# Performance work log

Measured on AMD Instinct MI355X. Metric: run time of the kernel, lower is better.

The kernel has to match this reference:

```python
import jax, jax.numpy as jnp
import numpy as np

LN_EPS = 1e-5  # torch nn.LayerNorm default


def _layernorm(h):
    # elementwise_affine=False LayerNorm over last dim
    mu = jnp.mean(h, axis=-1, keepdims=True)
    var = jnp.var(h, axis=-1, keepdims=True)
    return (h - mu) * jax.lax.rsqrt(var + LN_EPS)


def setup_inputs() -> dict:
    key = jax.random.key(0)
    ks = jax.random.split(key, 7)
    B, M, D, L = 10240, 8, 512, 3  # b=1024*10 and m=8 are hardcoded in the module
    rn = lambda k, shape, scale=1.0: jax.random.normal(k, shape, dtype=jnp.float32) * scale
    return {
        "x":   rn(ks[0], (B, D)),
        "Ws":  rn(ks[1], (L, M, D, D), 0.05),  # per-layer basis weight tensors (m,i,j)
        "bs":  rn(ks[2], (L, M, D), 0.05),     # per-layer basis biases (m,i)
        "pWs": rn(ks[3], (L, B, M)),           # per-sample weight-mixing coeffs
        "pbs": rn(ks[4], (L, B, M)),           # per-sample bias-mixing coeffs
        "gWs": rn(ks[5], (L, B, D, 1)),        # gates (squeezed in forward)
        "gbs": rn(ks[6], (L, B, D)),
    }


def reference(x, Ws, bs, pWs, pbs, gWs, gbs):
    L = Ws.shape[0]
    for l in range(L):
        gW = gWs[l][..., 0]                                  # (b, i)
        # 'bi,bm,mij,bj->bi' without materializing (b,i,j):
        y = jnp.einsum('mij,bj->bmi', Ws[l], x)              # (b, m, i)
        Wx = gW * jnp.einsum('bm,bmi->bi', pWs[l], y)        # (b, i)
        # 'bj,bm,mj->bj' (bias lives in output dim)
        bias = gbs[l] * jnp.einsum('bm,mi->bi', pbs[l], bs[l])
        h = Wx + bias
        if l != L - 1:  # hidden layers: LayerNorm (no affine) + ELU; last: identity
            h = jax.nn.elu(_layernorm(h))
        x = h
    return x
```

## Files before the change

kernel.cpp:

```cpp
#include <hip/hip_runtime.h>
#include <math.h>

#define BB   10240
#define DD   512
#define MM   8

typedef _Float16 h8 __attribute__((ext_vector_type(8)));
typedef float    f4 __attribute__((ext_vector_type(4)));

__device__ __forceinline__ void gload16(const void* g, void* l) {
    __builtin_amdgcn_global_load_lds(
        (__attribute__((address_space(1))) void*)(g),
        (__attribute__((address_space(3))) void*)(l), 16, 0, 0);
}

__global__ void __launch_bounds__(256) cvt_f32_f16(const float* __restrict__ s,
                                                   _Float16* __restrict__ d, int n8) {
    int i = blockIdx.x * 256 + threadIdx.x;
    if (i >= n8) return;
    const float4* sp = (const float4*)s + (size_t)i * 2;
    float4 a = sp[0], b = sp[1];
    h8 o = { (_Float16)a.x, (_Float16)a.y, (_Float16)a.z, (_Float16)a.w,
             (_Float16)b.x, (_Float16)b.y, (_Float16)b.z, (_Float16)b.w };
    *(h8*)(d + (size_t)i * 8) = o;
}

template <int HALF_OUT>
__global__ void __launch_bounds__(256, 3) gemm_layer(
    const _Float16* __restrict__ xh,
    const _Float16* __restrict__ Wh,
    const float*  __restrict__ pW,
    const float*  __restrict__ pb,
    const float*  __restrict__ bsv,
    const float*  __restrict__ gW,
    const float*  __restrict__ gb,
    float* __restrict__ outf,
    _Float16* __restrict__ outh)
{
    __shared__ __align__(16) _Float16 Wl[4][3][32 * 64];

    const int tid  = threadIdx.x;
    const int lane = tid & 63;
    const int w    = tid >> 6;
    const int wm   = w >> 1, wn = w & 1;
    const int ln16 = lane & 15, quad = lane >> 4;
    const int bn0  = blockIdx.x * 64;
    const int bm0  = blockIdx.y * 128;

    _Float16 pwh[4][8];
    #pragma unroll
    for (int mt = 0; mt < 4; ++mt) {
        const float* pp = pW + (size_t)(bm0 + wm * 64 + mt * 16 + ln16) * MM;
        float4 p0 = *(const float4*)pp;
        float4 p1 = *(const float4*)(pp + 4);
        pwh[mt][0] = (_Float16)p0.x; pwh[mt][1] = (_Float16)p0.y;
        pwh[mt][2] = (_Float16)p0.z; pwh[mt][3] = (_Float16)p0.w;
        pwh[mt][4] = (_Float16)p1.x; pwh[mt][5] = (_Float16)p1.y;
        pwh[mt][6] = (_Float16)p1.z; pwh[mt][7] = (_Float16)p1.w;
    }

    const _Float16* ab0 = xh + (size_t)(bm0 + wm * 64 + ln16) * DD + quad * 8;

    f4 acc[4][2] = {};
    h8 afr[2][4], afn[2][4];

#define STW(S_, M_, JC_) do {                                                  \
    _Pragma("unroll")                                                          \
    for (int c = 0; c < 4; ++c) {                                              \
        int rit     = c * 8 + (lane >> 3);             \
        int logical = (lane & 7) ^ (lane >> 3);           \
        const _Float16* gp = Wh + (size_t)(M_) * (DD * DD)                     \
                               + (size_t)(bn0 + wn * 32 + rit) * DD            \
                               + (JC_) * 64 + logical * 8;                     \
        gload16(gp, &Wl[w][S_][c * 512]);                                      \
    }                                                                          \
} while (0)

#define AL(DST, JC) do {                                                       \
    _Pragma("unroll")                                                          \
    for (int _ks = 0; _ks < 2; ++_ks)                                          \
        _Pragma("unroll")                                                      \
        for (int _mt = 0; _mt < 4; ++_mt)                                      \
            DST[_ks][_mt] = *(const h8*)(ab0 + (size_t)_mt * (16 * DD)         \
                                         + (size_t)(JC) * 64 + _ks * 32);      \
} while (0)

#define GS(T_, N_, CUR, NXT, DOA) do {                                         \
    if ((T_) + 2 <= 63) STW((((T_) + 2) % 3), (((T_) + 2) & 7),                \
                            (((T_) + 2) >> 3));                                \
    if (DOA) AL(NXT, ((T_) >> 3) + 1);                                         \
    asm volatile("s_waitcnt vmcnt(%0)" :: "i"(N_) : "memory");                 \
    __builtin_amdgcn_sched_barrier(0);                                         \
    h8 wfr[2][2];                                                              \
    _Pragma("unroll")                                                          \
    for (int ks = 0; ks < 2; ++ks)                                             \
        _Pragma("unroll")                                                      \
        for (int nt = 0; nt < 2; ++nt) {                                       \
            int row  = nt * 16 + ln16;                                         \
            int phys = (ks * 4 + quad) ^ (ln16 & 7);                           \
            wfr[ks][nt] = *(const h8*)&Wl[w][(T_) % 3][row * 64 + phys * 8];   \
        }                                                                      \
    _Pragma("unroll")                                                          \
    for (int ks = 0; ks < 2; ++ks)                                             \
        _Pragma("unroll")                                                      \
        for (int mt = 0; mt < 4; ++mt) {                                       \
            h8 as = CUR[ks][mt] * pwh[mt][(T_) & 7];      \
            acc[mt][0] = __builtin_amdgcn_mfma_f32_16x16x32_f16(               \
                as, wfr[ks][0], acc[mt][0], 0, 0, 0);                          \
            acc[mt][1] = __builtin_amdgcn_mfma_f32_16x16x32_f16(               \
                as, wfr[ks][1], acc[mt][1], 0, 0, 0);                          \
        }                                                                      \
} while (0)

    AL(afr, 0);
    STW(0, 0, 0);
    STW(1, 1, 0);

    GS( 0,  8, afr, afn, 0);            
    GS( 1,  8, afr, afn, 0);
    GS( 2,  8, afr, afn, 0);
    GS( 3, 16, afr, afn, 1);
    GS( 4, 16, afr, afn, 0);
    GS( 5, 16, afr, afn, 0);
    GS( 6,  8, afr, afn, 0);
    GS( 7,  8, afr, afn, 0);
    GS( 8,  8, afn, afr, 0);
    GS( 9,  8, afn, afr, 0);
    GS(10,  8, afn, afr, 0);
    GS(11, 16, afn, afr, 1);
    GS(12, 16, afn, afr, 0);
    GS(13, 16, afn, afr, 0);
    GS(14,  8, afn, afr, 0);
    GS(15,  8, afn, afr, 0);
    GS(16,  8, afr, afn, 0);
    GS(17,  8, afr, afn, 0);
    GS(18,  8, afr, afn, 0);
    GS(19, 16, afr, afn, 1);
    GS(20, 16, afr, afn, 0);
    GS(21, 16, afr, afn, 0);
    GS(22,  8, afr, afn, 0);
    GS(23,  8, afr, afn, 0);
    GS(24,  8, afn, afr, 0);
    GS(25,  8, afn, afr, 0);
    GS(26,  8, afn, afr, 0);
    GS(27, 16, afn, afr, 1);
    GS(28, 16, afn, afr, 0);
    GS(29, 16, afn, afr, 0);
    GS(30,  8, afn, afr, 0);
    GS(31,  8, afn, afr, 0);
    GS(32,  8, afr, afn, 0);
    GS(33,  8, afr, afn, 0);
    GS(34,  8, afr, afn, 0);
    GS(35, 16, afr, afn, 1);
    GS(36, 16, afr, afn, 0);
    GS(37, 16, afr, afn, 0);
    GS(38,  8, afr, afn, 0);
    GS(39,  8, afr, afn, 0);
    GS(40,  8, afn, afr, 0);
    GS(41,  8, afn, afr, 0);
    GS(42,  8, afn, afr, 0);
    GS(43, 16, afn, afr, 1);
    GS(44, 16, afn, afr, 0);
    GS(45, 16, afn, afr, 0);
    GS(46,  8, afn, afr, 0);
    GS(47,  8, afn, afr, 0);
    GS(48,  8, afr, afn, 0);
    GS(49,  8, afr, afn, 0);
    GS(50,  8, afr, afn, 0);
    GS(51, 16, afr, afn, 1);
    GS(52, 16, afr, afn, 0);
    GS(53, 16, afr, afn, 0);
    GS(54,  8, afr, afn, 0);
    GS(55,  8, afr, afn, 0);
    GS(56,  8, afn, afr, 0);
    GS(57,  8, afn, afr, 0);
    GS(58,  8, afn, afr, 0);
    GS(59,  8, afn, afr, 0);
    GS(60,  8, afn, afr, 0);
    GS(61,  8, afn, afr, 0);
    GS(62,  4, afn, afr, 0);
    GS(63,  0, afn, afr, 0);

#undef GS
#undef AL
#undef STW

    const int i0 = bn0 + wn * 32 + ln16;
    const int i1 = i0 + 16;
    float bs0[8], bs1[8];
    #pragma unroll
    for (int m2 = 0; m2 < 8; ++m2) {
        bs0[m2] = bsv[m2 * DD + i0];
        bs1[m2] = bsv[m2 * DD + i1];
    }
    #pragma unroll
    for (int mt = 0; mt < 4; ++mt) {
        #pragma unroll
        for (int r = 0; r < 4; ++r) {
            int b = bm0 + wm * 64 + mt * 16 + quad * 4 + r;
            float4 p0 = *(const float4*)(pb + (size_t)b * MM);
            float4 p1 = *(const float4*)(pb + (size_t)b * MM + 4);
            float bias0 = p0.x*bs0[0] + p0.y*bs0[1] + p0.z*bs0[2] + p0.w*bs0[3]
                        + p1.x*bs0[4] + p1.y*bs0[5] + p1.z*bs0[6] + p1.w*bs0[7];
            float bias1 = p0.x*bs1[0] + p0.y*bs1[1] + p0.z*bs1[2] + p0.w*bs1[3]
                        + p1.x*bs1[4] + p1.y*bs1[5] + p1.z*bs1[6] + p1.w*bs1[7];
            float v0 = gW[(size_t)b * DD + i0] * acc[mt][0][r] + gb[(size_t)b * DD + i0] * bias0;
            float v1 = gW[(size_t)b * DD + i1] * acc[mt][1][r] + gb[(size_t)b * DD + i1] * bias1;
            if (HALF_OUT) {
                outh[(size_t)b * DD + i0] = (_Float16)v0;
                outh[(size_t)b * DD + i1] = (_Float16)v1;
            } else {
                outf[(size_t)b * DD + i0] = v0;
                outf[(size_t)b * DD + i1] = v1;
            }
        }
    }
}

__global__ void __launch_bounds__(256) ln_elu_h(const _Float16* __restrict__ h,
                                                _Float16* __restrict__ xo) {
    const int w    = threadIdx.x >> 6;
    const int lane = threadIdx.x & 63;
    const int row  = blockIdx.x * 4 + w;
    h8 v = *(const h8*)(h + (size_t)row * DD + lane * 8);
    float f[8], s = 0.f, q = 0.f;
    #pragma unroll
    for (int i = 0; i < 8; ++i) { f[i] = (float)v[i]; s += f[i]; q += f[i] * f[i]; }
    #pragma unroll
    for (int off = 1; off < 64; off <<= 1) {
        s += __shfl_xor(s, off);
        q += __shfl_xor(q, off);
    }
    float mu   = s * (1.0f / 512.0f);
    float var  = q * (1.0f / 512.0f) - mu * mu;
    float rstd = rsqrtf(var + 1e-5f);
    h8 o;
    #pragma unroll
    for (int i = 0; i < 8; ++i) {
        float t = (f[i] - mu) * rstd;
        t = t > 0.0f ? t : expm1f(t);
        o[i] = (_Float16)t;
    }
    *(h8*)(xo + (size_t)row * DD + lane * 8) = o;
}

extern "C" void kernel_launch(void* const* d_in, const int* in_sizes, int n_in,
                              void* d_out, int out_size, void* d_ws, size_t ws_size,
                              hipStream_t stream) {
    const float* x   = (const float*)d_in[0];
    const float* Ws  = (const float*)d_in[1];
    const float* bs  = (const float*)d_in[2];
    const float* pWs = (const float*)d_in[3];
    const float* pbs = (const float*)d_in[4];
    const float* gWs = (const float*)d_in[5];
    const float* gbs = (const float*)d_in[6];
    float* out = (float*)d_out;

    _Float16* Wh = (_Float16*)d_ws;
    _Float16* xh = Wh + (size_t)3 * MM * DD * DD;
    _Float16* hh = xh + (size_t)BB * DD;

    const int wsl = MM * DD * DD;
    const int bsl = MM * DD;
    const int pl  = BB * MM;
    const int gl  = BB * DD;

    cvt_f32_f16<<<3072, 256, 0, stream>>>(Ws, Wh, 786432);
    cvt_f32_f16<<<2560, 256, 0, stream>>>(x, xh, 655360);

    dim3 gg(DD / 64, BB / 128);

    gemm_layer<1><<<gg, 256, 0, stream>>>(xh, Wh, pWs, pbs, bs, gWs, gbs,
                                          nullptr, hh);
    ln_elu_h<<<BB / 4, 256, 0, stream>>>(hh, xh);
    gemm_layer<1><<<gg, 256, 0, stream>>>(xh, Wh + wsl, pWs + pl, pbs + pl,
                                          bs + bsl, gWs + gl, gbs + gl,
                                          nullptr, hh);
    ln_elu_h<<<BB / 4, 256, 0, stream>>>(hh, xh);
    gemm_layer<0><<<gg, 256, 0, stream>>>(xh, Wh + 2 * wsl, pWs + 2 * pl,
                                          pbs + 2 * pl, bs + 2 * bsl,
                                          gWs + 2 * gl, gbs + 2 * gl,
                                          out, nullptr);
}
```

Measured before the change: 377.1 us.

## Use two waves per block, each computing 128x32 tile with single A buffer

Reorganizes the GEMM block from four waves (2x2 over a 128x64 tile) to two waves, each covering all 128 rows and a 32-column slice. Each wave loads A once and reuses it across twice as many MFMAs, and the A double buffer is dropped in favor of reloading after the eighth step of each chunk. This raises per-wave register use (accumulators for 8 row tiles) and lowers occupancy via launch bounds (128,2). It also exposes A load latency at chunk boundaries, since those loads are no longer prefetched ahead.

Result: no change. 374.5 us (-0.7%).

```diff
diff --git a/kernel.cpp b/kernel.cpp
--- a/kernel.cpp
+++ b/kernel.cpp
@@ -26,7 +26,7 @@
 }
 
 template <int HALF_OUT>
-__global__ void __launch_bounds__(256, 3) gemm_layer(
+__global__ void __launch_bounds__(128, 2) gemm_layer(
     const _Float16* __restrict__ xh,
     const _Float16* __restrict__ Wh,
     const float*  __restrict__ pW,
@@ -37,20 +37,19 @@
     float* __restrict__ outf,
     _Float16* __restrict__ outh)
 {
-    __shared__ __align__(16) _Float16 Wl[4][3][32 * 64];
+    __shared__ __align__(16) _Float16 Wl[2][3][32 * 64];
 
     const int tid  = threadIdx.x;
     const int lane = tid & 63;
     const int w    = tid >> 6;
-    const int wm   = w >> 1, wn = w & 1;
     const int ln16 = lane & 15, quad = lane >> 4;
     const int bn0  = blockIdx.x * 64;
     const int bm0  = blockIdx.y * 128;
 
-    _Float16 pwh[4][8];
-    #pragma unroll
-    for (int mt = 0; mt < 4; ++mt) {
-        const float* pp = pW + (size_t)(bm0 + wm * 64 + mt * 16 + ln16) * MM;
+    _Float16 pwh[8][8];
+    #pragma unroll
+    for (int mt = 0; mt < 8; ++mt) {
+        const float* pp = pW + (size_t)(bm0 + mt * 16 + ln16) * MM;
         float4 p0 = *(const float4*)pp;
         float4 p1 = *(const float4*)(pp + 4);
         pwh[mt][0] = (_Float16)p0.x; pwh[mt][1] = (_Float16)p0.y;
@@ -59,10 +58,10 @@
         pwh[mt][6] = (_Float16)p1.z; pwh[mt][7] = (_Float16)p1.w;
     }
 
-    const _Float16* ab0 = xh + (size_t)(bm0 + wm * 64 + ln16) * DD + quad * 8;
-
-    f4 acc[4][2] = {};
-    h8 afr[2][4], afn[2][4];
+    const _Float16* ab0 = xh + (size_t)(bm0 + ln16) * DD + quad * 8;
+
+    f4 acc[8][2] = {};
+    h8 afr[2][8];
 
 #define STW(S_, M_, JC_) do {                                                  \
     _Pragma("unroll")                                                          \
@@ -70,25 +69,24 @@
         int rit     = c * 8 + (lane >> 3);             \
         int logical = (lane & 7) ^ (lane >> 3);           \
         const _Float16* gp = Wh + (size_t)(M_) * (DD * DD)                     \
-                               + (size_t)(bn0 + wn * 32 + rit) * DD            \
+                               + (size_t)(bn0 + w * 32 + rit) * DD             \
                                + (JC_) * 64 + logical * 8;                     \
         gload16(gp, &Wl[w][S_][c * 512]);                                      \
     }                                                                          \
 } while (0)
 
-#define AL(DST, JC) do {                                                       \
+#define AL(JC) do {                                                            \
     _Pragma("unroll")                                                          \
     for (int _ks = 0; _ks < 2; ++_ks)                                          \
         _Pragma("unroll")                                                      \
-        for (int _mt = 0; _mt < 4; ++_mt)                                      \
-            DST[_ks][_mt] = *(const h8*)(ab0 + (size_t)_mt * (16 * DD)         \
+        for (int _mt = 0; _mt < 8; ++_mt)                                      \
+            afr[_ks][_mt] = *(const h8*)(ab0 + (size_t)_mt * (16 * DD)         \
                                          + (size_t)(JC) * 64 + _ks * 32);      \
 } while (0)
 
-#define GS(T_, N_, CUR, NXT, DOA) do {                                         \
+#define GS(T_, N_, PA_) do {                                                   \
     if ((T_) + 2 <= 63) STW((((T_) + 2) % 3), (((T_) + 2) & 7),                \
                             (((T_) + 2) >> 3));                                \
-    if (DOA) AL(NXT, ((T_) >> 3) + 1);                                         \
     asm volatile("s_waitcnt vmcnt(%0)" :: "i"(N_) : "memory");                 \
     __builtin_amdgcn_sched_barrier(0);                                         \
     h8 wfr[2][2];                                                              \
@@ -103,89 +101,42 @@
     _Pragma("unroll")                                                          \
     for (int ks = 0; ks < 2; ++ks)                                             \
         _Pragma("unroll")                                                      \
-        for (int mt = 0; mt < 4; ++mt) {                                       \
-            h8 as = CUR[ks][mt] * pwh[mt][(T_) & 7];      \
+        for (int mt = 0; mt < 8; ++mt) {                                       \
+            h8 as = afr[ks][mt] * pwh[mt][(T_) & 7];      \
             acc[mt][0] = __builtin_amdgcn_mfma_f32_16x16x32_f16(               \
                 as, wfr[ks][0], acc[mt][0], 0, 0, 0);                          \
             acc[mt][1] = __builtin_amdgcn_mfma_f32_16x16x32_f16(               \
                 as, wfr[ks][1], acc[mt][1], 0, 0, 0);                          \
         }                                                                      \
+    if (PA_) AL(((T_) >> 3) + 1);                                              \
 } while (0)
 
-    AL(afr, 0);
+    AL(0);
     STW(0, 0, 0);
     STW(1, 1, 0);
 
-    GS( 0,  8, afr, afn, 0);            
-    GS( 1,  8, afr, afn, 0);
-    GS( 2,  8, afr, afn, 0);
-    GS( 3, 16, afr, afn, 1);
-    GS( 4, 16, afr, afn, 0);
-    GS( 5, 16, afr, afn, 0);
-    GS( 6,  8, afr, afn, 0);
-    GS( 7,  8, afr, afn, 0);
-    GS( 8,  8, afn, afr, 0);
-    GS( 9,  8, afn, afr, 0);
-    GS(10,  8, afn, afr, 0);
-    GS(11, 16, afn, afr, 1);
-    GS(12, 16, afn, afr, 0);
-    GS(13, 16, afn, afr, 0);
-    GS(14,  8, afn, afr, 0);
-    GS(15,  8, afn, afr, 0);
-    GS(16,  8, afr, afn, 0);
-    GS(17,  8, afr, afn, 0);
-    GS(18,  8, afr, afn, 0);
-    GS(19, 16, afr, afn, 1);
-    GS(20, 16, afr, afn, 0);
-    GS(21, 16, afr, afn, 0);
-    GS(22,  8, afr, afn, 0);
-    GS(23,  8, afr, afn, 0);
-    GS(24,  8, afn, afr, 0);
-    GS(25,  8, afn, afr, 0);
-    GS(26,  8, afn, afr, 0);
-    GS(27, 16, afn, afr, 1);
-    GS(28, 16, afn, afr, 0);
-    GS(29, 16, afn, afr, 0);
-    GS(30,  8, afn, afr, 0);
-    GS(31,  8, afn, afr, 0);
-    GS(32,  8, afr, afn, 0);
-    GS(33,  8, afr, afn, 0);
-    GS(34,  8, afr, afn, 0);
-    GS(35, 16, afr, afn, 1);
-    GS(36, 16, afr, afn, 0);
-    GS(37, 16, afr, afn, 0);
-    GS(38,  8, afr, afn, 0);
-    GS(39,  8, afr, afn, 0);
-    GS(40,  8, afn, afr, 0);
-    GS(41,  8, afn, afr, 0);
-    GS(42,  8, afn, afr, 0);
-    GS(43, 16, afn, afr, 1);
-    GS(44, 16, afn, afr, 0);
-    GS(45, 16, afn, afr, 0);
-    GS(46,  8, afn, afr, 0);
-    GS(47,  8, afn, afr, 0);
-    GS(48,  8, afr, afn, 0);
-    GS(49,  8, afr, afn, 0);
-    GS(50,  8, afr, afn, 0);
-    GS(51, 16, afr, afn, 1);
-    GS(52, 16, afr, afn, 0);
-    GS(53, 16, afr, afn, 0);
-    GS(54,  8, afr, afn, 0);
-    GS(55,  8, afr, afn, 0);
-    GS(56,  8, afn, afr, 0);
-    GS(57,  8, afn, afr, 0);
-    GS(58,  8, afn, afr, 0);
-    GS(59,  8, afn, afr, 0);
-    GS(60,  8, afn, afr, 0);
-    GS(61,  8, afn, afr, 0);
-    GS(62,  4, afn, afr, 0);
-    GS(63,  0, afn, afr, 0);
+    GS( 0,  8, 0); GS( 1,  8, 0); GS( 2,  8, 0); GS( 3,  8, 0);
+    GS( 4,  8, 0); GS( 5,  8, 0); GS( 6,  8, 0); GS( 7,  8, 1);
+    GS( 8, 24, 0); GS( 9,  8, 0); GS(10,  8, 0); GS(11,  8, 0);
+    GS(12,  8, 0); GS(13,  8, 0); GS(14,  8, 0); GS(15,  8, 1);
+    GS(16, 24, 0); GS(17,  8, 0); GS(18,  8, 0); GS(19,  8, 0);
+    GS(20,  8, 0); GS(21,  8, 0); GS(22,  8, 0); GS(23,  8, 1);
+    GS(24, 24, 0); GS(25,  8, 0); GS(26,  8, 0); GS(27,  8, 0);
+    GS(28,  8, 0); GS(29,  8, 0); GS(30,  8, 0); GS(31,  8, 1);
+    GS(32, 24, 0); GS(33,  8, 0); GS(34,  8, 0); GS(35,  8, 0);
+    GS(36,  8, 0); GS(37,  8, 0); GS(38,  8, 0); GS(39,  8, 1);
+    GS(40, 24, 0); GS(41,  8, 0); GS(42,  8, 0); GS(43,  8, 0);
+    GS(44,  8, 0); GS(45,  8, 0); GS(46,  8, 0); GS(47,  8, 1);
+    GS(48, 24, 0); GS(49,  8, 0); GS(50,  8, 0); GS(51,  8, 0);
+    GS(52,  8, 0); GS(53,  8, 0); GS(54,  8, 0); GS(55,  8, 1);
+    GS(56, 24, 0); GS(57,  8, 0); GS(58,  8, 0); GS(59,  8, 0);
+    GS(60,  8, 0); GS(61,  8, 0); GS(62,  4, 0); GS(63,  0, 0);
 
 #undef GS
 #undef AL
 #undef STW
 
-    const int i0 = bn0 + wn * 32 + ln16;
+    const int i0 = bn0 + w * 32 + ln16;
     const int i1 = i0 + 16;
     float bs0[8], bs1[8];
     #pragma unroll
@@ -194,10 +145,10 @@
         bs1[m2] = bsv[m2 * DD + i1];
     }
     #pragma unroll
-    for (int mt = 0; mt < 4; ++mt) {
+    for (int mt = 0; mt < 8; ++mt) {
         #pragma unroll
         for (int r = 0; r < 4; ++r) {
-            int b = bm0 + wm * 64 + mt * 16 + quad * 4 + r;
+            int b = bm0 + mt * 16 + quad * 4 + r;
             float4 p0 = *(const float4*)(pb + (size_t)b * MM);
             float4 p1 = *(const float4*)(pb + (size_t)b * MM + 4);
             float bias0 = p0.x*bs0[0] + p0.y*bs0[1] + p0.z*bs0[2] + p0.w*bs0[3]
@@ -270,14 +221,14 @@
 
     dim3 gg(DD / 64, BB / 128);
 
-    gemm_layer<1><<<gg, 256, 0, stream>>>(xh, Wh, pWs, pbs, bs, gWs, gbs,
+    gemm_layer<1><<<gg, 128, 0, stream>>>(xh, Wh, pWs, pbs, bs, gWs, gbs,
                                           nullptr, hh);
     ln_elu_h<<<BB / 4, 256, 0, stream>>>(hh, xh);
-    gemm_layer<1><<<gg, 256, 0, stream>>>(xh, Wh + wsl, pWs + pl, pbs + pl,
+    gemm_layer<1><<<gg, 128, 0, stream>>>(xh, Wh + wsl, pWs + pl, pbs + pl,
                                           bs + bsl, gWs + gl, gbs + gl,
                                           nullptr, hh);
     ln_elu_h<<<BB / 4, 256, 0, stream>>>(hh, xh);
-    gemm_layer<0><<<gg, 256, 0, stream>>>(xh, Wh + 2 * wsl, pWs + 2 * pl,
+    gemm_layer<0><<<gg, 128, 0, stream>>>(xh, Wh + 2 * wsl, pWs + 2 * pl,
                                           pbs + 2 * pl, bs + 2 * bsl,
                                           gWs + 2 * gl, gbs + 2 * gl,
                                           out, nullptr);
```
